# Kernel tuning notes

Hardware: AMD Instinct MI355X
Metric: run time of the kernel (lower is better)

The kernel has to match this reference:

```python
import jax, jax.numpy as jnp
import numpy as np

B, C, H, W = 32, 128, 56, 56
O = 256
KH, KW = 3, 3
SH, SW = 1, 1
PH, PW = 1, 1
T = 6          # num_terms
R = 8          # low_rank
D = C * KH * KW          # 1152
R2 = R * KH * KW         # 72


def setup_inputs() -> dict:
    key = jax.random.key(0)
    ks = jax.random.split(key, 6)
    scale = 0.05
    return {
        "x": jax.random.normal(ks[0], (B, C, H, W), dtype=jnp.float32),
        "S1s": jax.random.normal(ks[1], (T, D, R), dtype=jnp.float32) * scale,
        "U1s": jax.random.normal(ks[2], (T, R, O), dtype=jnp.float32) * scale,
        "U2s": jax.random.normal(ks[3], (T, R2, D), dtype=jnp.float32) * scale,
        "S2s": jax.random.normal(ks[4], (T, R2, O), dtype=jnp.float32) * scale,
        "bias": jax.random.normal(ks[5], (O,), dtype=jnp.float32) * scale,
    }


def _extract_windows(x):
    # im2col: pad then gather strided windows; d flattened in (C, kh, kw) order
    xp = jnp.pad(x, ((0, 0), (0, 0), (PH, PH), (PW, PW)))
    Hp, Wp = xp.shape[2], xp.shape[3]
    Ho = (Hp - KH) // SH + 1
    Wo = (Wp - KW) // SW + 1
    # stack KH*KW shifted views -> [B, C, KH*KW, Ho, Wo]
    patches = jnp.stack(
        [xp[:, :, i:i + SH * Ho:SH, j:j + SW * Wo:SW]
         for i in range(KH) for j in range(KW)],
        axis=2,
    )
    # -> [B, Ho, Wo, C, KH*KW] -> [N, C*KH*KW]
    xw = patches.transpose(0, 3, 4, 1, 2).reshape(B * Ho * Wo, D)
    return xw, Ho, Wo


def reference(x, S1s, U1s, U2s, S2s, bias):
    xw, Ho, Wo = _extract_windows(x)                    # [N, D]
    # term 1: x_windows @ S1s[t] @ U1s[t], averaged over terms
    out1 = jnp.einsum('nd,tdr,tro->no', xw, S1s, U1s, optimize=True) / T + bias
    # term 2: x_windows @ U2s[t].T @ S2s[t], averaged over terms
    out2 = jnp.einsum('nd,tdr,tro->no', xw, jnp.swapaxes(U2s, 1, 2), S2s,
                      optimize=True) / T
    # NOTE: bias is added twice, faithfully matching the original module
    out = (out1 + out2 + bias).reshape(B, Ho, Wo, O).transpose(0, 3, 1, 2)
    return out
```

## Files before the change

kernel.cpp:

```cpp
#include <hip/hip_runtime.h>
#include <hip/hip_bf16.h>

typedef __attribute__((ext_vector_type(8))) short  short8;
typedef __attribute__((ext_vector_type(8))) unsigned short ushort8;
typedef __attribute__((ext_vector_type(4))) unsigned short usv4;
typedef __attribute__((ext_vector_type(4))) float  f32x4;

#define D_DIM 1152
#define O_DIM 256
#define N_TOT 100352
#define XT_H 58
#define XT_ROW (58 * 128)

__device__ __forceinline__ unsigned short f2bf(float f) {
  __hip_bfloat16 h = __float2bfloat16(f);
  return __builtin_bit_cast(unsigned short, h);
}

#define GLOAD_LDS16(g, l)                                              \
  __builtin_amdgcn_global_load_lds(                                    \
      (const __attribute__((address_space(1))) void*)(g),              \
      (__attribute__((address_space(3))) void*)(l), 16, 0, 0)

__global__ __launch_bounds__(256) void wt_kernel(
    const float* __restrict__ S1s, const float* __restrict__ U1s,
    const float* __restrict__ U2s, const float* __restrict__ S2s,
    unsigned short* __restrict__ Wt) {
  __shared__ float A_lds[32][64];
  __shared__ float B_lds[32][64];

  const int bo = blockIdx.x & 3;
  const int bd = blockIdx.x >> 2;
  const int o0  = bo << 6;
  const int dn0 = bd << 6;
  const int rr  = dn0 >> 7;
  const int c0  = dn0 & 127;

  const int tid = threadIdx.x;
  const int ty = tid >> 4, tx = tid & 15;

  float acc[4][4] = {};

  for (int kc = 0; kc < 15; ++kc) {
#pragma unroll
    for (int e = 0; e < 8; ++e) {
      const int li = e * 256 + tid;
      const int kk = li >> 6;
      const int xx = li & 63;
      const int k  = kc * 32 + kk;
      float av, bv;
      if (k < 48) {
        av = U1s[k * O_DIM + o0 + xx];
        const int d_old = (c0 + xx) * 9 + rr;
        bv = S1s[(size_t)((k >> 3) * D_DIM + d_old) * 8 + (k & 7)];
      } else {
        const int kq = k - 48;
        av = S2s[(size_t)kq * O_DIM + o0 + xx];
        const int d_old = (c0 + xx) * 9 + rr;
        bv = U2s[(size_t)kq * D_DIM + d_old];
      }
      A_lds[kk][xx] = av;
      B_lds[kk][xx] = bv;
    }
    __syncthreads();
#pragma unroll
    for (int kk = 0; kk < 32; ++kk) {
      f32x4 a = *(const f32x4*)&A_lds[kk][ty << 2];
      f32x4 b = *(const f32x4*)&B_lds[kk][tx << 2];
#pragma unroll
      for (int i = 0; i < 4; ++i)
#pragma unroll
        for (int j = 0; j < 4; ++j)
          acc[i][j] += a[i] * b[j];
    }
    __syncthreads();
  }

#pragma unroll
  for (int i = 0; i < 4; ++i) {
    usv4 v;
#pragma unroll
    for (int j = 0; j < 4; ++j) v[j] = f2bf(acc[i][j] * (1.0f / 6.0f));
    *(usv4*)(Wt + (size_t)(o0 + (ty << 2) + i) * D_DIM + dn0 + (tx << 2)) = v;
  }
}

__global__ __launch_bounds__(256) void pad_kernel(const float* __restrict__ x,
                                                  unsigned short* __restrict__ xt) {
  int blk = blockIdx.x;
  int b = blk / XT_H, ih = blk - b * XT_H;
  unsigned short* dst = xt + (size_t)blk * XT_ROW;
  int tid = threadIdx.x;

  if (ih == 0 || ih == XT_H - 1) {
    ushort8 z;
#pragma unroll
    for (int q = 0; q < 8; ++q) z[q] = 0;
    for (int i = tid; i < XT_ROW / 8; i += 256) ((ushort8*)dst)[i] = z;
    return;
  }

  __shared__ unsigned short lds[128 * 58];
  int h = ih - 1;
  const float* xb = x + (size_t)b * 128 * 3136 + (size_t)h * 56;
#pragma unroll 4
  for (int r = 0; r < 28; ++r) {
    int idx = r * 256 + tid;
    int c = idx / 56, w2 = idx - c * 56;
    lds[c * 58 + w2] = f2bf(xb[(size_t)c * 3136 + w2]);
  }
  __syncthreads();
#pragma unroll 4
  for (int r = 0; r < 29; ++r) {
    int idx = r * 256 + tid;
    int iw = idx >> 7, c = idx & 127;
    unsigned short v = 0;
    if (iw >= 1 && iw <= 56) v = lds[c * 58 + (iw - 1)];
    dst[idx] = v;
  }
}

__device__ __forceinline__ constexpr int KB_OFF(int kt) {
  int rr = kt >> 1;
  return ((rr / 3) * 58 + (rr % 3)) * 128 + (kt & 1) * 64;
}

#define ST_A(kts, sl2, r) \
  GLOAD_LDS16(pA[r] + (kts) * 64, smem + (sl2) * 24576 + (r) * 4096 + (w << 9))
#define ST_B(kts, sl2, r) \
  GLOAD_LDS16(pB[r] + KB_OFF(kts), smem + (sl2) * 24576 + 8192 + (r) * 4096 + (w << 9))

#define LDS_FRAG(base, row, ks)                                            \
  (*(const short8*)((const char*)(base) +                                  \
     ((((row) * 128) + (ks) * 64 + ((lane >> 4) << 4)) ^ ((((row) >> 2) & 1) << 5))))

__global__ __launch_bounds__(512, 2) void gemm_kernel(
    const unsigned short* __restrict__ Wt, const unsigned short* __restrict__ xt,
    const float* __restrict__ bias, float* __restrict__ out) {
  __shared__ __align__(1024) unsigned short smem[3 * 24576];

  const int bid   = blockIdx.x;
  const int lid   = (bid & 7) * 98 + (bid >> 3);
  const int ntile = lid >> 1, otile = lid & 1;
  const int n0 = ntile << 8;
  const int o0 = otile << 7;

  const int tid  = threadIdx.x;
  const int w    = tid >> 6;
  const int lane = tid & 63;
  const int wm   = w >> 2;
  const int wn   = w & 3;

  const unsigned short* pA[2];
  const unsigned short* pB[4];
#pragma unroll
  for (int r = 0; r < 2; ++r) {
    const int li  = r * 512 + tid;
    const int row = li >> 3;
    const int gs  = (li & 7) ^ (((row >> 2) & 1) << 1);
    pA[r] = Wt + (size_t)(o0 + row) * D_DIM + gs * 8;
  }
#pragma unroll
  for (int r = 0; r < 4; ++r) {
    const int li  = r * 512 + tid;
    const int row = li >> 3;
    const int gs  = (li & 7) ^ (((row >> 2) & 1) << 1);
    const int n_g = n0 + row;
    const int b   = n_g / 3136;
    const int s   = n_g - b * 3136;
    const int oh  = s / 56, ow = s - oh * 56;
    pB[r] = xt + (((size_t)b * XT_H + oh) * XT_H + ow) * 128 + gs * 8;
  }

  f32x4 acc[4][4] = {};

  ST_A(0, 0, 0); ST_A(0, 0, 1);
  ST_B(0, 0, 0); ST_B(0, 0, 1); ST_B(0, 0, 2); ST_B(0, 0, 3);
  ST_A(1, 1, 0); ST_A(1, 1, 1);
  ST_B(1, 1, 0); ST_B(1, 1, 1); ST_B(1, 1, 2); ST_B(1, 1, 3);
  asm volatile("s_waitcnt vmcnt(6)" ::: "memory");
  __builtin_amdgcn_s_barrier();

#pragma unroll
  for (int kt = 0; kt < 18; ++kt) {
    const int sl  = kt % 3;
    const int kts = kt + 2;
    const int sl2 = kts % 3;
    const unsigned short* As = smem + sl * 24576;
    const unsigned short* Bs = smem + sl * 24576 + 8192;

    short8 af[4][2], bf[2][2], bf2[2][2];

#pragma unroll
    for (int mi = 0; mi < 4; ++mi) {
      const int row = (wm << 6) + (mi << 4) + (lane & 15);
      af[mi][0] = LDS_FRAG(As, row, 0);
      af[mi][1] = LDS_FRAG(As, row, 1);
    }
#pragma unroll
    for (int ni = 0; ni < 2; ++ni) {
      const int row = (wn << 6) + (ni << 4) + (lane & 15);
      bf[ni][0] = LDS_FRAG(Bs, row, 0);
      bf[ni][1] = LDS_FRAG(Bs, row, 1);
    }
    if (kts < 18) { ST_A(kts, sl2, 0); ST_A(kts, sl2, 1); ST_B(kts, sl2, 0); }
    __builtin_amdgcn_s_barrier();
    __builtin_amdgcn_s_setprio(1);
#pragma unroll
    for (int mi = 0; mi < 4; ++mi)
#pragma unroll
      for (int ni = 0; ni < 2; ++ni)
#pragma unroll
        for (int ks = 0; ks < 2; ++ks)
          acc[mi][ni] = __builtin_amdgcn_mfma_f32_16x16x32_bf16(
              af[mi][ks], bf[ni][ks], acc[mi][ni], 0, 0, 0);
    __builtin_amdgcn_s_setprio(0);
    __builtin_amdgcn_s_barrier();

#pragma unroll
    for (int ni = 0; ni < 2; ++ni) {
      const int row = (wn << 6) + ((ni + 2) << 4) + (lane & 15);
      bf2[ni][0] = LDS_FRAG(Bs, row, 0);
      bf2[ni][1] = LDS_FRAG(Bs, row, 1);
    }
    if (kts < 18) { ST_B(kts, sl2, 1); ST_B(kts, sl2, 2); ST_B(kts, sl2, 3); }
    __builtin_amdgcn_s_barrier();
    __builtin_amdgcn_s_setprio(1);
#pragma unroll
    for (int mi = 0; mi < 4; ++mi)
#pragma unroll
      for (int ni = 0; ni < 2; ++ni)
#pragma unroll
        for (int ks = 0; ks < 2; ++ks)
          acc[mi][2 + ni] = __builtin_amdgcn_mfma_f32_16x16x32_bf16(
              af[mi][ks], bf2[ni][ks], acc[mi][2 + ni], 0, 0, 0);
    __builtin_amdgcn_s_setprio(0);
    if (kt < 16) asm volatile("s_waitcnt vmcnt(6)" ::: "memory");
    else         asm volatile("s_waitcnt vmcnt(0)" ::: "memory");
    __builtin_amdgcn_s_barrier();
  }

  const int lr = (lane >> 4) << 2;
  const int lc = lane & 15;
#pragma unroll
  for (int ni = 0; ni < 4; ++ni) {
    const int ng = n0 + (wn << 6) + (ni << 4) + lc;
    const int b  = ng / 3136;
    const int s  = ng - b * 3136;
    float* op = out + (size_t)b * (O_DIM * 3136) + s;
#pragma unroll
    for (int mi = 0; mi < 4; ++mi) {
      const int og = o0 + (wm << 6) + (mi << 4) + lr;
#pragma unroll
      for (int r = 0; r < 4; ++r)
        op[(size_t)(og + r) * 3136] = acc[mi][ni][r] + 2.0f * bias[og + r];
    }
  }
}

extern "C" void kernel_launch(void* const* d_in, const int* in_sizes, int n_in,
                              void* d_out, int out_size, void* d_ws, size_t ws_size,
                              hipStream_t stream) {
  const float* x    = (const float*)d_in[0];
  const float* S1s  = (const float*)d_in[1];
  const float* U1s  = (const float*)d_in[2];
  const float* U2s  = (const float*)d_in[3];
  const float* S2s  = (const float*)d_in[4];
  const float* bias = (const float*)d_in[5];
  float* out = (float*)d_out;
  (void)ws_size;

  unsigned short* xt = (unsigned short*)d_ws;
  unsigned short* Wt = (unsigned short*)((char*)d_ws + (size_t)32 * XT_H * XT_ROW * 2);

  pad_kernel<<<dim3(32 * XT_H), dim3(256), 0, stream>>>(x, xt);
  wt_kernel<<<dim3(72), dim3(256), 0, stream>>>(S1s, U1s, U2s, S2s, Wt);
  gemm_kernel<<<dim3(784), dim3(512), 0, stream>>>(Wt, xt, bias, out);
}
```

Baseline: 138.8 us.

## Use full 8-way XOR LDS swizzle and merge split K-step into one phase

```diff
diff --git a/kernel.cpp b/kernel.cpp
--- a/kernel.cpp
+++ b/kernel.cpp
@@ -131,8 +131,8 @@
   GLOAD_LDS16(pB[r] + KB_OFF(kts), smem + (sl2) * 24576 + 8192 + (r) * 4096 + (w << 9))
 
 #define LDS_FRAG(base, row, ks)                                            \
-  (*(const short8*)((const char*)(base) +                                  \
-     ((((row) * 128) + (ks) * 64 + ((lane >> 4) << 4)) ^ ((((row) >> 2) & 1) << 5))))
+  (*(const short8*)((const char*)(base) + (row) * 128 +                    \
+     (((((ks) << 2) + (lane >> 4)) ^ ((row) & 7)) << 4)))
 
 __global__ __launch_bounds__(512, 2) void gemm_kernel(
     const unsigned short* __restrict__ Wt, const unsigned short* __restrict__ xt,
@@ -157,14 +157,14 @@
   for (int r = 0; r < 2; ++r) {
     const int li  = r * 512 + tid;
     const int row = li >> 3;
-    const int gs  = (li & 7) ^ (((row >> 2) & 1) << 1);
+    const int gs  = (li & 7) ^ (row & 7);
     pA[r] = Wt + (size_t)(o0 + row) * D_DIM + gs * 8;
   }
 #pragma unroll
   for (int r = 0; r < 4; ++r) {
     const int li  = r * 512 + tid;
     const int row = li >> 3;
-    const int gs  = (li & 7) ^ (((row >> 2) & 1) << 1);
+    const int gs  = (li & 7) ^ (row & 7);
     const int n_g = n0 + row;
     const int b   = n_g / 3136;
     const int s   = n_g - b * 3136;
@@ -189,8 +189,7 @@
     const unsigned short* As = smem + sl * 24576;
     const unsigned short* Bs = smem + sl * 24576 + 8192;
 
-    short8 af[4][2], bf[2][2], bf2[2][2];
-
+    short8 af[4][2], bf[4][2];
 #pragma unroll
     for (int mi = 0; mi < 4; ++mi) {
       const int row = (wm << 6) + (mi << 4) + (lane & 15);
@@ -198,42 +197,24 @@
       af[mi][1] = LDS_FRAG(As, row, 1);
     }
 #pragma unroll
-    for (int ni = 0; ni < 2; ++ni) {
+    for (int ni = 0; ni < 4; ++ni) {
       const int row = (wn << 6) + (ni << 4) + (lane & 15);
       bf[ni][0] = LDS_FRAG(Bs, row, 0);
       bf[ni][1] = LDS_FRAG(Bs, row, 1);
     }
-    if (kts < 18) { ST_A(kts, sl2, 0); ST_A(kts, sl2, 1); ST_B(kts, sl2, 0); }
-    __builtin_amdgcn_s_barrier();
+    if (kts < 18) {
+      ST_A(kts, sl2, 0); ST_A(kts, sl2, 1);
+      ST_B(kts, sl2, 0); ST_B(kts, sl2, 1); ST_B(kts, sl2, 2); ST_B(kts, sl2, 3);
+    }
     __builtin_amdgcn_s_setprio(1);
 #pragma unroll
-    for (int mi = 0; mi < 4; ++mi)
-#pragma unroll
-      for (int ni = 0; ni < 2; ++ni)
-#pragma unroll
-        for (int ks = 0; ks < 2; ++ks)
+    for (int ks = 0; ks < 2; ++ks)
+#pragma unroll
+      for (int mi = 0; mi < 4; ++mi)
+#pragma unroll
+        for (int ni = 0; ni < 4; ++ni)
           acc[mi][ni] = __builtin_amdgcn_mfma_f32_16x16x32_bf16(
               af[mi][ks], bf[ni][ks], acc[mi][ni], 0, 0, 0);
-    __builtin_amdgcn_s_setprio(0);
-    __builtin_amdgcn_s_barrier();
-
-#pragma unroll
-    for (int ni = 0; ni < 2; ++ni) {
-      const int row = (wn << 6) + ((ni + 2) << 4) + (lane & 15);
-      bf2[ni][0] = LDS_FRAG(Bs, row, 0);
-      bf2[ni][1] = LDS_FRAG(Bs, row, 1);
-    }
-    if (kts < 18) { ST_B(kts, sl2, 1); ST_B(kts, sl2, 2); ST_B(kts, sl2, 3); }
-    __builtin_amdgcn_s_barrier();
-    __builtin_amdgcn_s_setprio(1);
-#pragma unroll
-    for (int mi = 0; mi < 4; ++mi)
-#pragma unroll
-      for (int ni = 0; ni < 2; ++ni)
-#pragma unroll
-        for (int ks = 0; ks < 2; ++ks)
-          acc[mi][2 + ni] = __builtin_amdgcn_mfma_f32_16x16x32_bf16(
-              af[mi][ks], bf2[ni][ks], acc[mi][2 + ni], 0, 0, 0);
     __builtin_amdgcn_s_setprio(0);
     if (kt < 16) asm volatile("s_waitcnt vmcnt(6)" ::: "memory");
     else         asm volatile("s_waitcnt vmcnt(0)" ::: "memory");
```

Result: faster. 126.4 us (-9.0%).
